# Kernel tuning notes

Hardware: AMD Instinct MI355X
Metric: run time of the kernel (lower is better)

## Reference

```python
import jax, jax.numpy as jnp
import numpy as np

CUTOFF = 5.0
EPS = 1e-7
N = 50000
L = 160.0


def _cart3(a, b, c):
    # cartesian product of ranges [-a..a] x [-b..b] x [-c..c], row-major like torch.cartesian_prod
    A, B, C = np.meshgrid(np.arange(-a, a + 1), np.arange(-b, b + 1), np.arange(-c, c + 1), indexing='ij')
    return np.stack([A.ravel(), B.ravel(), C.ravel()], axis=1)


def wrap_positions(positions, cell):
    scaled = positions @ jnp.linalg.inv(cell) + EPS
    scaled = scaled % 1.0 - EPS
    return scaled @ cell


def setup_inputs() -> dict:
    key = jax.random.key(0)
    positions = jax.random.uniform(key, (N, 3), dtype=jnp.float32) * L
    cell = jnp.eye(3, dtype=jnp.float32) * L
    return {"positions": positions, "cell": cell}


def reference(positions, cell):
    wrapped = wrap_positions(positions, cell)

    cell_np = np.asarray(cell, dtype=np.float64)
    norm_a = np.linalg.norm(np.cross(cell_np[1], cell_np[2]))
    norm_b = np.linalg.norm(np.cross(cell_np[2], cell_np[0]))
    norm_c = np.linalg.norm(np.cross(cell_np[0], cell_np[1]))
    volume = float(np.dot(cell_np[0], np.cross(cell_np[1], cell_np[2])))
    pa = int(np.ceil(CUTOFF * norm_a / volume))
    pb = int(np.ceil(CUTOFF * norm_b / volume))
    pc = int(np.ceil(CUTOFF * norm_c / volume))

    pad_mat = jnp.asarray(_cart3(pa, pb, pc), dtype=positions.dtype)  # [P,3]
    P = pad_mat.shape[0]
    n = wrapped.shape[0]

    # replicate atoms into all periodic images: index k -> atom k//P, image k%P
    padded_pos = (wrapped[:, None, :] + pad_mat @ cell).reshape(-1, 3)  # [n*P,3]
    padded_cpos = jnp.floor(padded_pos / CUTOFF).astype(jnp.int32)
    corner = padded_cpos.min(axis=0)
    padded_cpos = padded_cpos - corner
    shap = np.asarray(padded_cpos.max(axis=0)) + 1
    num_cells = int(shap.prod())
    count_vec = jnp.asarray([int(shap[1] * shap[2]), int(shap[2]), 1], dtype=jnp.int32)

    padded_cind = (padded_cpos * count_vec).sum(axis=1)  # linear cell id per padded atom
    padded_gind = jnp.arange(n * P, dtype=jnp.int32) + 1  # 1-based so 0 == empty slot
    padded_rind = jnp.repeat(jnp.arange(n, dtype=jnp.int32), P)  # real-atom id of each image

    atom_cpos = jnp.floor(wrapped / CUTOFF).astype(jnp.int32) - corner
    disp = jnp.asarray(_cart3(1, 1, 1), dtype=jnp.int32)  # 27-cell stencil
    atom_cnind = ((atom_cpos[:, None, :] + disp) * count_vec).sum(axis=-1)  # [n,27]

    # stable sort by cell id, then within-cell rank (== torch unique_consecutive bookkeeping)
    cind_np = np.asarray(padded_cind)
    order = np.argsort(cind_np, kind='stable')
    sorted_cind = cind_np[order]
    _, counts = np.unique(sorted_cind, return_counts=True)
    max_anum = int(counts.max())
    starts = np.repeat(np.cumsum(counts) - counts, counts)
    ranks = np.arange(sorted_cind.shape[0]) - starts

    gci = jnp.zeros((num_cells, max_anum, 2), dtype=jnp.int32)
    gci = gci.at[sorted_cind, ranks, 0].set(padded_gind[order])
    gci = gci.at[sorted_cind, ranks, 1].set(padded_rind[order])

    atom_nind = gci[atom_cnind]  # [n,27,max_anum,2]
    occ = np.asarray(atom_nind[..., 0])
    pair_i, neigh, jslot = np.nonzero(occ)
    pair_jp = occ[pair_i, neigh, jslot] - 1  # index into padded_pos
    pair_j = np.asarray(atom_nind[..., 1])[pair_i, neigh, jslot]

    pair_diff = padded_pos[pair_jp] - wrapped[pair_i]
    pair_dist = jnp.linalg.norm(pair_diff, axis=1)
    mask = np.asarray((pair_dist < CUTOFF) & (pair_dist > 0.01))
    keep = np.nonzero(mask)[0]

    pairs = jnp.stack([jnp.asarray(pair_i, jnp.int32), jnp.asarray(pair_j, jnp.int32)], axis=1)
    return pairs[keep], pair_diff[keep], pair_dist[keep]
```

## Files before the change

### kernel.cpp

```cpp
#include <hip/hip_runtime.h>
#include <hip/hip_bf16.h>


#define CUTOFF 5.0f
#define WEPS   1e-7f
#define PIMG   27
#define G      36
#define NCELLS (G*G*G)
#define SLOT   16
#define NBLK   256
#define NTHR   1024
#define TOTT   (NBLK*NTHR)
#define JPT    6
#define PCH    (NTHR*JPT)
#define CAP    12
#define CSTR   13
#define NGRP   16
#define BPG    (NBLK/NGRP)
#define GSTR   64
#define IMAX   0x7FFFFFFF
#define SPINCAP (1<<20)
#define PRUNE2 25.001f

__device__ __forceinline__ void gsync(int* grp, int* top, int* rel, int phase) {
  __syncthreads();
  if (threadIdx.x == 0) {
    __threadfence();
    int g = blockIdx.x & (NGRP - 1);
    if (__hip_atomic_fetch_add(&grp[g * GSTR], 1, __ATOMIC_RELEASE,
                               __HIP_MEMORY_SCOPE_AGENT) == BPG * phase - 1) {
      if (__hip_atomic_fetch_add(top, 1, __ATOMIC_RELEASE,
                                 __HIP_MEMORY_SCOPE_AGENT) == NGRP * phase - 1) {
        __hip_atomic_store(rel, phase, __ATOMIC_RELEASE, __HIP_MEMORY_SCOPE_SYSTEM);
      }
    }
    int guard = 0;
    while (__hip_atomic_load(rel, __ATOMIC_RELAXED, __HIP_MEMORY_SCOPE_SYSTEM) < phase) {
      __builtin_amdgcn_s_sleep(8);
      if (++guard > SPINCAP) break;
    }
    __threadfence();
  }
  __syncthreads();
}

__device__ __forceinline__ int block_exscan(int v, int* lds, int* total) {
  int tid = threadIdx.x, lane = tid & 63, wave = tid >> 6;
  int x = v;
#pragma unroll
  for (int off = 1; off < 64; off <<= 1) {
    int y = __shfl_up(x, off);
    if (lane >= off) x += y;
  }
  if (lane == 63) lds[wave] = x;
  __syncthreads();
  if (wave == 0) {
    int wv = (lane < 16) ? lds[lane] : 0;
#pragma unroll
    for (int off = 1; off < 16; off <<= 1) {
      int y = __shfl_up(wv, off);
      if (lane >= off) wv += y;
    }
    if (lane < 16) lds[lane] = wv;
  }
  __syncthreads();
  int wbase = (wave == 0) ? 0 : lds[wave - 1];
  *total = lds[15];
  __syncthreads();
  return wbase + x - v;
}

__device__ __forceinline__ void inv_diag3(const float* __restrict__ cell, float inv[9]) {
  float c[9];
#pragma unroll
  for (int i = 0; i < 9; i++) c[i] = cell[i];
  float a00=c[0],a01=c[1],a02=c[2],a10=c[3],a11=c[4],a12=c[5],a20=c[6],a21=c[7],a22=c[8];
  float m00 = __fsub_rn(__fmul_rn(a11,a22), __fmul_rn(a12,a21));
  float m01 = __fsub_rn(__fmul_rn(a10,a22), __fmul_rn(a12,a20));
  float m02 = __fsub_rn(__fmul_rn(a10,a21), __fmul_rn(a11,a20));
  float det = __fadd_rn(__fsub_rn(__fmul_rn(a00,m00), __fmul_rn(a01,m01)), __fmul_rn(a02,m02));
  inv[0] = __fdiv_rn(m00, det);
  inv[1] = __fdiv_rn(__fsub_rn(__fmul_rn(a02,a21), __fmul_rn(a01,a22)), det);
  inv[2] = __fdiv_rn(__fsub_rn(__fmul_rn(a01,a12), __fmul_rn(a02,a11)), det);
  inv[3] = __fdiv_rn(__fsub_rn(__fmul_rn(a12,a20), __fmul_rn(a10,a22)), det);
  inv[4] = __fdiv_rn(__fsub_rn(__fmul_rn(a00,a22), __fmul_rn(a02,a20)), det);
  inv[5] = __fdiv_rn(__fsub_rn(__fmul_rn(a02,a10), __fmul_rn(a00,a12)), det);
  inv[6] = __fdiv_rn(m02, det);
  inv[7] = __fdiv_rn(__fsub_rn(__fmul_rn(a01,a20), __fmul_rn(a00,a21)), det);
  inv[8] = __fdiv_rn(__fsub_rn(__fmul_rn(a00,a11), __fmul_rn(a01,a10)), det);
}

__device__ __forceinline__ int axis_opts(float w, float cdiag, int* pcomp, int* cellv,
                                         float* shv) {
  int cc = (int)floorf(__fdiv_rn(w, CUTOFF));
  int k = 0;
  if (cc >= 29) {
    float wp = __fsub_rn(w, cdiag);
    int c2 = (int)floorf(__fdiv_rn(wp, CUTOFF)) + 2;
    if ((unsigned)c2 < G) { pcomp[k] = 0; cellv[k] = c2; shv[k] = __fsub_rn(0.0f, cdiag); k++; }
  }
  pcomp[k] = 1; cellv[k] = cc + 2; shv[k] = 0.0f; k++;
  if (cc <= 2) {
    float wp = __fadd_rn(w, cdiag);
    int c2 = (int)floorf(__fdiv_rn(wp, CUTOFF)) + 2;
    if ((unsigned)c2 < G) { pcomp[k] = 2; cellv[k] = c2; shv[k] = cdiag; k++; }
  }
  return k;
}

__device__ __forceinline__ bool dist_ok(float4 f, float4 w) {
  float ax = __fsub_rn(f.x, w.x), ay = __fsub_rn(f.y, w.y), az = __fsub_rn(f.z, w.z);
  float d = __fsqrt_rn(__fadd_rn(__fadd_rn(__fmul_rn(ax, ax), __fmul_rn(ay, ay)),
                                 __fmul_rn(az, az)));
  return (d < CUTOFF && d > 0.01f);
}

__device__ __forceinline__ unsigned match_mask(const float4* __restrict__ cdata,
                                               int base, int cnt, float4 w) {
  unsigned mask = 0;
  for (int q = 0; q < cnt; q++)
    if (dist_ok(cdata[base + q], w)) mask |= 1u << q;
  return mask;
}

__device__ __forceinline__ int pick_min_t(const float4* __restrict__ cdata, int base,
                                          unsigned mask) {
  int bq = -1, bt = IMAX;
  for (unsigned m2 = mask; m2; m2 &= m2 - 1) {
    int q = __builtin_ctz(m2);
    int t = __float_as_int(cdata[base + q].w);
    if (t < bt) { bt = t; bq = q; }
  }
  return bq;
}

__device__ __forceinline__ float axis_q(float w, int c) {
  float lo = (float)((c - 2) * 5);
  float t = w - lo;
  float v = fmaxf(fmaxf(-t, t - 5.0f), 0.0f);
  return v * v;
}

__device__ __forceinline__ void cswap(int& a, int& b) {
  int lo = min(a, b), hi = max(a, b);
  a = lo; b = hi;
}

__global__ void __launch_bounds__(NTHR)
k_fused(const float* __restrict__ pos, const float* __restrict__ cell,
        float* __restrict__ out, int n, int K,
        int* grp, int* top, int* rel, int* fill,
        float4* wrapped, int* pubSum, float4* cdata) {
  __shared__ int lds[32];
  __shared__ int pcache[NTHR * CSTR];
  const int tid = threadIdx.x, blk = blockIdx.x;
  const int n27 = n * PIMG;

  const int CH = (n + NBLK - 1) / NBLK;
  const int ai = blk * CH + tid;
  if (tid < CH && ai < n) {
    float inv[9];
    inv_diag3(cell, inv);
    float px = pos[3*ai], py = pos[3*ai+1], pz = pos[3*ai+2];
    float m[3];
#pragma unroll
    for (int col = 0; col < 3; col++) {
      float s = __fadd_rn(__fadd_rn(__fmul_rn(px, inv[col]), __fmul_rn(py, inv[3+col])),
                          __fmul_rn(pz, inv[6+col]));
      s = __fadd_rn(s, WEPS);
      float t = __fsub_rn(s, floorf(s));
      m[col] = __fsub_rn(t, WEPS);
    }
    float wx = __fadd_rn(__fadd_rn(__fmul_rn(m[0], cell[0]), __fmul_rn(m[1], cell[3])),
                         __fmul_rn(m[2], cell[6]));
    float wy = __fadd_rn(__fadd_rn(__fmul_rn(m[0], cell[1]), __fmul_rn(m[1], cell[4])),
                         __fmul_rn(m[2], cell[7]));
    float wz = __fadd_rn(__fadd_rn(__fmul_rn(m[0], cell[2]), __fmul_rn(m[1], cell[5])),
                         __fmul_rn(m[2], cell[8]));
    wrapped[ai] = make_float4(wx, wy, wz, 0.0f);
    int px_[2], py_[2], pz_[2], cx_[2], cy_[2], cz_[2];
    float sx_[2], sy_[2], sz_[2];
    int nx = axis_opts(wx, cell[0], px_, cx_, sx_);
    int ny = axis_opts(wy, cell[4], py_, cy_, sy_);
    int nz = axis_opts(wz, cell[8], pz_, cz_, sz_);
    for (int a = 0; a < nx; a++)
      for (int b = 0; b < ny; b++)
        for (int c = 0; c < nz; c++) {
          int cid = (cx_[a] * G + cy_[b]) * G + cz_[c];
          int p = (px_[a] * 3 + py_[b]) * 3 + pz_[c];
          int slot = atomicAdd(&fill[cid], 1);
          if (slot < SLOT)
            cdata[cid * SLOT + slot] =
                make_float4(__fadd_rn(wx, sx_[a]), __fadd_rn(wy, sy_[b]),
                            __fadd_rn(wz, sz_[c]), __int_as_float(ai * PIMG + p));
        }
  }
  gsync(grp, top, rel, 1);

  const int tbase = blk * PCH + tid * JPT;
  const int i0 = min(tbase, n27 - 1) / PIMG;
  const int i1 = min(tbase + JPT - 1, n27 - 1) / PIMG;
  const float4 w0 = wrapped[i0];
  const float4 w1 = wrapped[i1];
  const int cx0 = (int)floorf(__fdiv_rn(w0.x, CUTOFF)) + 2;
  const int cy0 = (int)floorf(__fdiv_rn(w0.y, CUTOFF)) + 2;
  const int cz0 = (int)floorf(__fdiv_rn(w0.z, CUTOFF)) + 2;
  const int cx1 = (int)floorf(__fdiv_rn(w1.x, CUTOFF)) + 2;
  const int cy1 = (int)floorf(__fdiv_rn(w1.y, CUTOFF)) + 2;
  const int cz1 = (int)floorf(__fdiv_rn(w1.z, CUTOFF)) + 2;
  int bases[JPT], cnts[JPT];
#pragma unroll
  for (int j = 0; j < JPT; j++) {
    int idx = tbase + j;
    bool valid = idx < n27;
    int ic = valid ? idx / PIMG : i0;
    int s27 = valid ? idx - ic * PIMG : 0;
    bool a0 = (ic == i0);
    int ix = s27 / 9, iy = (s27 / 3) % 3, iz = s27 % 3;
    float wxs = a0 ? w0.x : w1.x, wys = a0 ? w0.y : w1.y, wzs = a0 ? w0.z : w1.z;
    int cx = (a0 ? cx0 : cx1) + ix - 1;
    int cy = (a0 ? cy0 : cy1) + iy - 1;
    int cz = (a0 ? cz0 : cz1) + iz - 1;
    float ps = axis_q(wxs, cx) + axis_q(wys, cy) + axis_q(wzs, cz);
    bool keep = valid && (ps <= PRUNE2);
    int cid = (cx * G + cy) * G + cz;
    bases[j] = cid * SLOT;
    cnts[j] = keep ? min(fill[cid], SLOT) : 0;
  }
  int tcnt = 0, c0 = 0;
#pragma unroll
  for (int j = 0; j < JPT; j++) {
    bool a0 = (tbase + j) < (i0 + 1) * PIMG;
    float4 w = a0 ? w0 : w1;
    int base = bases[j], cnt = cnts[j];
    if (cnt > 0) {
      if (cnt <= 4) {
        float4 f0 = cdata[base + 0];
        float4 f1 = cdata[base + 1];
        float4 f2 = cdata[base + 2];
        float4 f3 = cdata[base + 3];
        int a = (cnt > 0 && dist_ok(f0, w)) ? (__float_as_int(f0.w) * 16 + 0) : IMAX;
        int b = (cnt > 1 && dist_ok(f1, w)) ? (__float_as_int(f1.w) * 16 + 1) : IMAX;
        int c = (cnt > 2 && dist_ok(f2, w)) ? (__float_as_int(f2.w) * 16 + 2) : IMAX;
        int d = (cnt > 3 && dist_ok(f3, w)) ? (__float_as_int(f3.w) * 16 + 3) : IMAX;
        cswap(a, b); cswap(c, d); cswap(a, c); cswap(b, d); cswap(b, c);
        if (a != IMAX) { if (tcnt < CAP) pcache[tid * CSTR + tcnt] = base + (a & 15); tcnt++; }
        if (b != IMAX) { if (tcnt < CAP) pcache[tid * CSTR + tcnt] = base + (b & 15); tcnt++; }
        if (c != IMAX) { if (tcnt < CAP) pcache[tid * CSTR + tcnt] = base + (c & 15); tcnt++; }
        if (d != IMAX) { if (tcnt < CAP) pcache[tid * CSTR + tcnt] = base + (d & 15); tcnt++; }
      } else {
        unsigned mask = match_mask(cdata, base, cnt, w);
        while (mask) {
          int bq = pick_min_t(cdata, base, mask);
          mask &= ~(1u << bq);
          if (tcnt < CAP) pcache[tid * CSTR + tcnt] = base + bq;
          tcnt++;
        }
      }
    }
    if (a0) c0 = tcnt;
  }
  int btotal;
  const int texcl = block_exscan(tcnt, lds, &btotal);

  if (tid == 0)
    __hip_atomic_store(&pubSum[blk], btotal + 1, __ATOMIC_RELAXED,
                       __HIP_MEMORY_SCOPE_SYSTEM);
  int v = 0;
  if (tid < NBLK) {
    int guard = 0;
    while ((v = __hip_atomic_load(&pubSum[tid], __ATOMIC_RELAXED,
                                  __HIP_MEMORY_SCOPE_SYSTEM)) == 0) {
      __builtin_amdgcn_s_sleep(2);
      if (++guard > SPINCAP) break;
    }
    v -= 1;
  }
  int obase, M;
  {
    int total;
    int ex = block_exscan(v, lds, &total);
    if (tid == blk) lds[16] = ex;
    if (tid == 0)   lds[17] = total;
    __syncthreads();
    obase = lds[16];
    M = lds[17];
  }

  if (blk == 0 && tid == 0 && M != K) {
    float code = (M < K) ? (1000000.0f + (float)min(K - M, 100000))
                         : (2000000.0f + (float)min(M - K, 100000));
    for (int t = 0; t < 256; t++) out[t] = code;
  }
  int o = texcl + obase;
  if (tcnt <= CAP) {
    for (int k = 0; k < tcnt; k++) {
      float4 f = cdata[pcache[tid * CSTR + k]];
      bool a0 = (k < c0);
      float4 w = a0 ? w0 : w1;
      int i = a0 ? i0 : i1;
      float ax = __fsub_rn(f.x, w.x), ay = __fsub_rn(f.y, w.y), az = __fsub_rn(f.z, w.z);
      float d = __fsqrt_rn(__fadd_rn(__fadd_rn(__fmul_rn(ax, ax), __fmul_rn(ay, ay)),
                                     __fmul_rn(az, az)));
      if (o >= 0 && o < K) {
        int tt = __float_as_int(f.w);
        ((float2*)out)[o] = make_float2((float)i, (float)(tt / PIMG));
        size_t db = (size_t)2 * K + (size_t)3 * o;
        out[db]     = ax;
        out[db + 1] = ay;
        out[db + 2] = az;
        out[(size_t)5 * K + o] = d;
      }
      o++;
    }
  } else {
#pragma unroll
    for (int j = 0; j < JPT; j++) {
      bool a0 = (tbase + j) < (i0 + 1) * PIMG;
      float4 w = a0 ? w0 : w1;
      int i = a0 ? i0 : i1;
      int base = bases[j];
      unsigned mask = match_mask(cdata, base, cnts[j], w);
      while (mask) {
        int bq = pick_min_t(cdata, base, mask);
        mask &= ~(1u << bq);
        float4 f = cdata[base + bq];
        float ax = __fsub_rn(f.x, w.x), ay = __fsub_rn(f.y, w.y), az = __fsub_rn(f.z, w.z);
        float d = __fsqrt_rn(__fadd_rn(__fadd_rn(__fmul_rn(ax, ax), __fmul_rn(ay, ay)),
                                       __fmul_rn(az, az)));
        if (o >= 0 && o < K) {
          int tt = __float_as_int(f.w);
          ((float2*)out)[o] = make_float2((float)i, (float)(tt / PIMG));
          size_t db = (size_t)2 * K + (size_t)3 * o;
          out[db]     = ax;
          out[db + 1] = ay;
          out[db + 2] = az;
          out[(size_t)5 * K + o] = d;
        }
        o++;
      }
    }
  }
}

extern "C" void kernel_launch(void* const* d_in, const int* in_sizes, int n_in,
                              void* d_out, int out_size, void* d_ws, size_t ws_size,
                              hipStream_t stream) {
  const float* pos  = (const float*)d_in[0];
  const float* cell = (const float*)d_in[1];
  float* out = (float*)d_out;
  int n = in_sizes[0] / 3;
  int K = out_size / 6;

  char* ws = (char*)d_ws;
  size_t off = 0;
  auto alloc = [&](size_t bytes) -> char* {
    char* p = ws + off;
    off = (off + bytes + 255) & ~(size_t)255;
    return p;
  };
  int*    grp      = (int*)alloc((size_t)NGRP * GSTR * 4);
  int*    top      = (int*)alloc(256);
  int*    rel      = (int*)alloc(256);
  int*    pubSum   = (int*)alloc((size_t)NBLK * 4);
  int*    fill     = (int*)alloc((size_t)NCELLS * 4);
  size_t  zbytes   = off;
  float4* wrapped  = (float4*)alloc((size_t)n * 16);
  float4* cdata    = (float4*)alloc((size_t)NCELLS * SLOT * 16);
  if (off > ws_size) return;

  (void)hipMemsetAsync(ws, 0, zbytes, stream);
  k_fused<<<NBLK, NTHR, 0, stream>>>(pos, cell, out, n, K, grp, top, rel, fill,
                                     wrapped, pubSum, cdata);
}
```

Baseline: 122.1 us.

## Split persistent fused kernel into build, pair, scan and emit kernels

Replaces the single persistent kernel, which used hand-rolled grid barriers and spin-waits on published block sums, with four ordinary launches: cell-list build, per-block pair discovery into a staging buffer, a single-block scan of block totals, and an emit pass that writes the outputs. This removes the spin-wait synchronisation and uses smaller 256-thread blocks with fewer items per thread, which should improve occupancy. In exchange it adds launch overhead for three extra kernels and a round trip through global memory for the staged pair addresses. NB2 and BCAP are fixed constants, so correctness depends on n*27 fitting within 2048*256*3 and on no block producing more than 512 pairs.

```diff
diff --git a/kernel.cpp b/kernel.cpp
--- a/kernel.cpp
+++ b/kernel.cpp
@@ -1,5 +1,4 @@
 #include <hip/hip_runtime.h>
-#include <hip/hip_bf16.h>
 
 
 #define CUTOFF 5.0f
@@ -8,67 +7,16 @@
 #define G      36
 #define NCELLS (G*G*G)
 #define SLOT   16
-#define NBLK   256
-#define NTHR   1024
-#define TOTT   (NBLK*NTHR)
-#define JPT    6
-#define PCH    (NTHR*JPT)
-#define CAP    12
-#define CSTR   13
-#define NGRP   16
-#define BPG    (NBLK/NGRP)
-#define GSTR   64
+#define NT1    256
+#define NB2    2048
+#define NT2    256
+#define JPT    3
+#define CAP    16
+#define CSTR   17
+#define BCAP   512
 #define IMAX   0x7FFFFFFF
-#define SPINCAP (1<<20)
 #define PRUNE2 25.001f
 
-__device__ __forceinline__ void gsync(int* grp, int* top, int* rel, int phase) {
-  __syncthreads();
-  if (threadIdx.x == 0) {
-    __threadfence();
-    int g = blockIdx.x & (NGRP - 1);
-    if (__hip_atomic_fetch_add(&grp[g * GSTR], 1, __ATOMIC_RELEASE,
-                               __HIP_MEMORY_SCOPE_AGENT) == BPG * phase - 1) {
-      if (__hip_atomic_fetch_add(top, 1, __ATOMIC_RELEASE,
-                                 __HIP_MEMORY_SCOPE_AGENT) == NGRP * phase - 1) {
-        __hip_atomic_store(rel, phase, __ATOMIC_RELEASE, __HIP_MEMORY_SCOPE_SYSTEM);
-      }
-    }
-    int guard = 0;
-    while (__hip_atomic_load(rel, __ATOMIC_RELAXED, __HIP_MEMORY_SCOPE_SYSTEM) < phase) {
-      __builtin_amdgcn_s_sleep(8);
-      if (++guard > SPINCAP) break;
-    }
-    __threadfence();
-  }
-  __syncthreads();
-}
-
-__device__ __forceinline__ int block_exscan(int v, int* lds, int* total) {
-  int tid = threadIdx.x, lane = tid & 63, wave = tid >> 6;
-  int x = v;
-#pragma unroll
-  for (int off = 1; off < 64; off <<= 1) {
-    int y = __shfl_up(x, off);
-    if (lane >= off) x += y;
-  }
-  if (lane == 63) lds[wave] = x;
-  __syncthreads();
-  if (wave == 0) {
-    int wv = (lane < 16) ? lds[lane] : 0;
-#pragma unroll
-    for (int off = 1; off < 16; off <<= 1) {
-      int y = __shfl_up(wv, off);
-      if (lane >= off) wv += y;
-    }
-    if (lane < 16) lds[lane] = wv;
-  }
-  __syncthreads();
-  int wbase = (wave == 0) ? 0 : lds[wave - 1];
-  *total = lds[15];
-  __syncthreads();
-  return wbase + x - v;
-}
 
 __device__ __forceinline__ void inv_diag3(const float* __restrict__ cell, float inv[9]) {
   float c[9];
@@ -146,58 +94,110 @@
   a = lo; b = hi;
 }
 
-__global__ void __launch_bounds__(NTHR)
-k_fused(const float* __restrict__ pos, const float* __restrict__ cell,
-        float* __restrict__ out, int n, int K,
-        int* grp, int* top, int* rel, int* fill,
-        float4* wrapped, int* pubSum, float4* cdata) {
-  __shared__ int lds[32];
-  __shared__ int pcache[NTHR * CSTR];
+__device__ __forceinline__ int exscan256(int v, int* lds, int* total) {
+  int tid = threadIdx.x, lane = tid & 63, wave = tid >> 6;
+  int x = v;
+#pragma unroll
+  for (int off = 1; off < 64; off <<= 1) {
+    int y = __shfl_up(x, off);
+    if (lane >= off) x += y;
+  }
+  if (lane == 63) lds[wave] = x;
+  __syncthreads();
+  if (wave == 0) {
+    int wv = (lane < 4) ? lds[lane] : 0;
+#pragma unroll
+    for (int off = 1; off < 4; off <<= 1) {
+      int y = __shfl_up(wv, off);
+      if (lane >= off) wv += y;
+    }
+    if (lane < 4) lds[lane] = wv;
+  }
+  __syncthreads();
+  int wbase = (wave == 0) ? 0 : lds[wave - 1];
+  *total = lds[3];
+  __syncthreads();
+  return wbase + x - v;
+}
+
+__device__ __forceinline__ int exscan1024(int v, int* lds, int* total) {
+  int tid = threadIdx.x, lane = tid & 63, wave = tid >> 6;
+  int x = v;
+#pragma unroll
+  for (int off = 1; off < 64; off <<= 1) {
+    int y = __shfl_up(x, off);
+    if (lane >= off) x += y;
+  }
+  if (lane == 63) lds[wave] = x;
+  __syncthreads();
+  if (wave == 0) {
+    int wv = (lane < 16) ? lds[lane] : 0;
+#pragma unroll
+    for (int off = 1; off < 16; off <<= 1) {
+      int y = __shfl_up(wv, off);
+      if (lane >= off) wv += y;
+    }
+    if (lane < 16) lds[lane] = wv;
+  }
+  __syncthreads();
+  int wbase = (wave == 0) ? 0 : lds[wave - 1];
+  *total = lds[15];
+  __syncthreads();
+  return wbase + x - v;
+}
+
+__global__ void __launch_bounds__(NT1)
+k_build(const float* __restrict__ pos, const float* __restrict__ cell,
+        int* __restrict__ fill, float4* __restrict__ wrapped,
+        float4* __restrict__ cdata, int n) {
+  const int ai = blockIdx.x * NT1 + threadIdx.x;
+  if (ai >= n) return;
+  float inv[9];
+  inv_diag3(cell, inv);
+  float px = pos[3*ai], py = pos[3*ai+1], pz = pos[3*ai+2];
+  float m[3];
+#pragma unroll
+  for (int col = 0; col < 3; col++) {
+    float s = __fadd_rn(__fadd_rn(__fmul_rn(px, inv[col]), __fmul_rn(py, inv[3+col])),
+                        __fmul_rn(pz, inv[6+col]));
+    s = __fadd_rn(s, WEPS);
+    float t = __fsub_rn(s, floorf(s));
+    m[col] = __fsub_rn(t, WEPS);
+  }
+  float wx = __fadd_rn(__fadd_rn(__fmul_rn(m[0], cell[0]), __fmul_rn(m[1], cell[3])),
+                       __fmul_rn(m[2], cell[6]));
+  float wy = __fadd_rn(__fadd_rn(__fmul_rn(m[0], cell[1]), __fmul_rn(m[1], cell[4])),
+                       __fmul_rn(m[2], cell[7]));
+  float wz = __fadd_rn(__fadd_rn(__fmul_rn(m[0], cell[2]), __fmul_rn(m[1], cell[5])),
+                       __fmul_rn(m[2], cell[8]));
+  wrapped[ai] = make_float4(wx, wy, wz, 0.0f);
+  int px_[2], py_[2], pz_[2], cx_[2], cy_[2], cz_[2];
+  float sx_[2], sy_[2], sz_[2];
+  int nx = axis_opts(wx, cell[0], px_, cx_, sx_);
+  int ny = axis_opts(wy, cell[4], py_, cy_, sy_);
+  int nz = axis_opts(wz, cell[8], pz_, cz_, sz_);
+  for (int a = 0; a < nx; a++)
+    for (int b = 0; b < ny; b++)
+      for (int c = 0; c < nz; c++) {
+        int cid = (cx_[a] * G + cy_[b]) * G + cz_[c];
+        int p = (px_[a] * 3 + py_[b]) * 3 + pz_[c];
+        int slot = atomicAdd(&fill[cid], 1);
+        if (slot < SLOT)
+          cdata[cid * SLOT + slot] =
+              make_float4(__fadd_rn(wx, sx_[a]), __fadd_rn(wy, sy_[b]),
+                          __fadd_rn(wz, sz_[c]), __int_as_float(ai * PIMG + p));
+      }
+}
+
+__global__ void __launch_bounds__(NT2)
+k_pair(const float4* __restrict__ wrapped, const int* __restrict__ fill,
+       const float4* __restrict__ cdata, int2* __restrict__ paddr,
+       int* __restrict__ blockSum, int n) {
+  __shared__ int lds[8];
+  __shared__ int pcache[NT2 * CSTR];
   const int tid = threadIdx.x, blk = blockIdx.x;
   const int n27 = n * PIMG;
-
-  const int CH = (n + NBLK - 1) / NBLK;
-  const int ai = blk * CH + tid;
-  if (tid < CH && ai < n) {
-    float inv[9];
-    inv_diag3(cell, inv);
-    float px = pos[3*ai], py = pos[3*ai+1], pz = pos[3*ai+2];
-    float m[3];
-#pragma unroll
-    for (int col = 0; col < 3; col++) {
-      float s = __fadd_rn(__fadd_rn(__fmul_rn(px, inv[col]), __fmul_rn(py, inv[3+col])),
-                          __fmul_rn(pz, inv[6+col]));
-      s = __fadd_rn(s, WEPS);
-      float t = __fsub_rn(s, floorf(s));
-      m[col] = __fsub_rn(t, WEPS);
-    }
-    float wx = __fadd_rn(__fadd_rn(__fmul_rn(m[0], cell[0]), __fmul_rn(m[1], cell[3])),
-                         __fmul_rn(m[2], cell[6]));
-    float wy = __fadd_rn(__fadd_rn(__fmul_rn(m[0], cell[1]), __fmul_rn(m[1], cell[4])),
-                         __fmul_rn(m[2], cell[7]));
-    float wz = __fadd_rn(__fadd_rn(__fmul_rn(m[0], cell[2]), __fmul_rn(m[1], cell[5])),
-                         __fmul_rn(m[2], cell[8]));
-    wrapped[ai] = make_float4(wx, wy, wz, 0.0f);
-    int px_[2], py_[2], pz_[2], cx_[2], cy_[2], cz_[2];
-    float sx_[2], sy_[2], sz_[2];
-    int nx = axis_opts(wx, cell[0], px_, cx_, sx_);
-    int ny = axis_opts(wy, cell[4], py_, cy_, sy_);
-    int nz = axis_opts(wz, cell[8], pz_, cz_, sz_);
-    for (int a = 0; a < nx; a++)
-      for (int b = 0; b < ny; b++)
-        for (int c = 0; c < nz; c++) {
-          int cid = (cx_[a] * G + cy_[b]) * G + cz_[c];
-          int p = (px_[a] * 3 + py_[b]) * 3 + pz_[c];
-          int slot = atomicAdd(&fill[cid], 1);
-          if (slot < SLOT)
-            cdata[cid * SLOT + slot] =
-                make_float4(__fadd_rn(wx, sx_[a]), __fadd_rn(wy, sy_[b]),
-                            __fadd_rn(wz, sz_[c]), __int_as_float(ai * PIMG + p));
-        }
-  }
-  gsync(grp, top, rel, 1);
-
-  const int tbase = blk * PCH + tid * JPT;
+  const int tbase = (blk * NT2 + tid) * JPT;
   const int i0 = min(tbase, n27 - 1) / PIMG;
   const int i1 = min(tbase + JPT - 1, n27 - 1) / PIMG;
   const float4 w0 = wrapped[i0];
@@ -261,59 +261,16 @@
     if (a0) c0 = tcnt;
   }
   int btotal;
-  const int texcl = block_exscan(tcnt, lds, &btotal);
-
-  if (tid == 0)
-    __hip_atomic_store(&pubSum[blk], btotal + 1, __ATOMIC_RELAXED,
-                       __HIP_MEMORY_SCOPE_SYSTEM);
-  int v = 0;
-  if (tid < NBLK) {
-    int guard = 0;
-    while ((v = __hip_atomic_load(&pubSum[tid], __ATOMIC_RELAXED,
-                                  __HIP_MEMORY_SCOPE_SYSTEM)) == 0) {
-      __builtin_amdgcn_s_sleep(2);
-      if (++guard > SPINCAP) break;
-    }
-    v -= 1;
-  }
-  int obase, M;
-  {
-    int total;
-    int ex = block_exscan(v, lds, &total);
-    if (tid == blk) lds[16] = ex;
-    if (tid == 0)   lds[17] = total;
-    __syncthreads();
-    obase = lds[16];
-    M = lds[17];
-  }
-
-  if (blk == 0 && tid == 0 && M != K) {
-    float code = (M < K) ? (1000000.0f + (float)min(K - M, 100000))
-                         : (2000000.0f + (float)min(M - K, 100000));
-    for (int t = 0; t < 256; t++) out[t] = code;
-  }
-  int o = texcl + obase;
+  const int texcl = exscan256(tcnt, lds, &btotal);
+  if (tid == 0) blockSum[blk] = btotal;
+  int2* dst = paddr + (size_t)blk * BCAP;
   if (tcnt <= CAP) {
     for (int k = 0; k < tcnt; k++) {
-      float4 f = cdata[pcache[tid * CSTR + k]];
-      bool a0 = (k < c0);
-      float4 w = a0 ? w0 : w1;
-      int i = a0 ? i0 : i1;
-      float ax = __fsub_rn(f.x, w.x), ay = __fsub_rn(f.y, w.y), az = __fsub_rn(f.z, w.z);
-      float d = __fsqrt_rn(__fadd_rn(__fadd_rn(__fmul_rn(ax, ax), __fmul_rn(ay, ay)),
-                                     __fmul_rn(az, az)));
-      if (o >= 0 && o < K) {
-        int tt = __float_as_int(f.w);
-        ((float2*)out)[o] = make_float2((float)i, (float)(tt / PIMG));
-        size_t db = (size_t)2 * K + (size_t)3 * o;
-        out[db]     = ax;
-        out[db + 1] = ay;
-        out[db + 2] = az;
-        out[(size_t)5 * K + o] = d;
-      }
-      o++;
+      int o = texcl + k;
+      if (o < BCAP) dst[o] = make_int2(pcache[tid * CSTR + k], (k < c0) ? i0 : i1);
     }
   } else {
+    int o = texcl;
 #pragma unroll
     for (int j = 0; j < JPT; j++) {
       bool a0 = (tbase + j) < (i0 + 1) * PIMG;
@@ -324,21 +281,54 @@
       while (mask) {
         int bq = pick_min_t(cdata, base, mask);
         mask &= ~(1u << bq);
-        float4 f = cdata[base + bq];
-        float ax = __fsub_rn(f.x, w.x), ay = __fsub_rn(f.y, w.y), az = __fsub_rn(f.z, w.z);
-        float d = __fsqrt_rn(__fadd_rn(__fadd_rn(__fmul_rn(ax, ax), __fmul_rn(ay, ay)),
-                                       __fmul_rn(az, az)));
-        if (o >= 0 && o < K) {
-          int tt = __float_as_int(f.w);
-          ((float2*)out)[o] = make_float2((float)i, (float)(tt / PIMG));
-          size_t db = (size_t)2 * K + (size_t)3 * o;
-          out[db]     = ax;
-          out[db + 1] = ay;
-          out[db + 2] = az;
-          out[(size_t)5 * K + o] = d;
-        }
+        if (o < BCAP) dst[o] = make_int2(base + bq, i);
         o++;
       }
+    }
+  }
+}
+
+__global__ void __launch_bounds__(1024)
+k_scan(const int* __restrict__ blockSum, int* __restrict__ blockBase,
+       float* __restrict__ out, int K) {
+  __shared__ int lds[32];
+  const int tid = threadIdx.x;
+  int s0 = blockSum[2 * tid], s1 = blockSum[2 * tid + 1];
+  int total;
+  int ex = exscan1024(s0 + s1, lds, &total);
+  blockBase[2 * tid] = ex;
+  blockBase[2 * tid + 1] = ex + s0;
+  if (tid == 0 && total != K) {
+    float code = (total < K) ? (1000000.0f + (float)min(K - total, 100000))
+                             : (2000000.0f + (float)min(total - K, 100000));
+    for (int t = 0; t < 256; t++) out[t] = code;
+  }
+}
+
+__global__ void __launch_bounds__(NT2)
+k_emit(const float4* __restrict__ wrapped, const float4* __restrict__ cdata,
+       const int2* __restrict__ paddr, const int* __restrict__ blockSum,
+       const int* __restrict__ blockBase, float* __restrict__ out, int K) {
+  const int blk = blockIdx.x;
+  const int bs = min(blockSum[blk], BCAP);
+  const int base = blockBase[blk];
+  const int2* src = paddr + (size_t)blk * BCAP;
+  for (int l = threadIdx.x; l < bs; l += NT2) {
+    int2 e = src[l];
+    float4 f = cdata[e.x];
+    float4 w = wrapped[e.y];
+    int o = base + l;
+    float ax = __fsub_rn(f.x, w.x), ay = __fsub_rn(f.y, w.y), az = __fsub_rn(f.z, w.z);
+    float d = __fsqrt_rn(__fadd_rn(__fadd_rn(__fmul_rn(ax, ax), __fmul_rn(ay, ay)),
+                                   __fmul_rn(az, az)));
+    if (o >= 0 && o < K) {
+      int tt = __float_as_int(f.w);
+      ((float2*)out)[o] = make_float2((float)e.y, (float)(tt / PIMG));
+      size_t db = (size_t)2 * K + (size_t)3 * o;
+      out[db]     = ax;
+      out[db + 1] = ay;
+      out[db + 2] = az;
+      out[(size_t)5 * K + o] = d;
     }
   }
 }
@@ -359,17 +349,19 @@
     off = (off + bytes + 255) & ~(size_t)255;
     return p;
   };
-  int*    grp      = (int*)alloc((size_t)NGRP * GSTR * 4);
-  int*    top      = (int*)alloc(256);
-  int*    rel      = (int*)alloc(256);
-  int*    pubSum   = (int*)alloc((size_t)NBLK * 4);
-  int*    fill     = (int*)alloc((size_t)NCELLS * 4);
-  size_t  zbytes   = off;
-  float4* wrapped  = (float4*)alloc((size_t)n * 16);
-  float4* cdata    = (float4*)alloc((size_t)NCELLS * SLOT * 16);
+  int*    fill      = (int*)alloc((size_t)NCELLS * 4);
+  size_t  zbytes    = off;
+  float4* wrapped   = (float4*)alloc((size_t)n * 16);
+  float4* cdata     = (float4*)alloc((size_t)NCELLS * SLOT * 16);
+  int2*   paddr     = (int2*)alloc((size_t)NB2 * BCAP * 8);
+  int*    blockSum  = (int*)alloc((size_t)NB2 * 4);
+  int*    blockBase = (int*)alloc((size_t)NB2 * 4);
   if (off > ws_size) return;
 
-  (void)hipMemsetAsync(ws, 0, zbytes, stream);
-  k_fused<<<NBLK, NTHR, 0, stream>>>(pos, cell, out, n, K, grp, top, rel, fill,
-                                     wrapped, pubSum, cdata);
-}
+  (void)hipMemsetAsync(fill, 0, zbytes, stream);
+  int nb1 = (n + NT1 - 1) / NT1;
+  k_build<<<nb1, NT1, 0, stream>>>(pos, cell, fill, wrapped, cdata, n);
+  k_pair<<<NB2, NT2, 0, stream>>>(wrapped, fill, cdata, paddr, blockSum, n);
+  k_scan<<<1, 1024, 0, stream>>>(blockSum, blockBase, out, K);
+  k_emit<<<NB2, NT2, 0, stream>>>(wrapped, cdata, paddr, blockSum, blockBase, out, K);
+}
```

Measured after the change: 98.63 us (median of 2 runs). 19.2% less time.
